# Kernel optimization log

Hardware: AMD Instinct MI355X
Metric: run time of the kernel (lower is better)

Reference implementation:

```python
import jax, jax.numpy as jnp
import numpy as np

DIM = 256
RED = DIM // 8  # reduction_ratio = 8
B, H, W = 16, 128, 128


def setup_inputs() -> dict:
    key = jax.random.key(0)
    ks = jax.random.split(key, 8)
    s = 1.0 / np.sqrt(DIM)  # conv2d default init scale (kernel_size=1 -> fan_in=dim)
    return {
        "x": jax.random.normal(ks[0], (B, DIM, H, W), dtype=jnp.float32),
        "y": jax.random.normal(ks[1], (B, DIM, H, W), dtype=jnp.float32),
        "q_w": jax.random.uniform(ks[2], (RED, DIM), jnp.float32, -s, s),
        "q_b": jax.random.uniform(ks[3], (RED,), jnp.float32, -s, s),
        "k_w": jax.random.uniform(ks[4], (RED, DIM), jnp.float32, -s, s),
        "k_b": jax.random.uniform(ks[5], (RED,), jnp.float32, -s, s),
        "v_w": jax.random.uniform(ks[6], (DIM, DIM), jnp.float32, -s, s),
        "v_b": jax.random.uniform(ks[7], (DIM,), jnp.float32, -s, s),
        "gamma": jnp.zeros((1,), dtype=jnp.float32),
    }


def reference(x, y, q_w, q_b, k_w, k_b, v_w, v_b, gamma):
    b, c, h, w = x.shape
    n = h * w
    # 1x1 convs are per-pixel channel GEMMs
    q = (jnp.einsum('bchw,oc->bohw', x, q_w) + q_b[None, :, None, None]).reshape(b, -1, n)
    k = (jnp.einsum('bchw,oc->bohw', y, k_w) + k_b[None, :, None, None]).reshape(b, -1, n)
    v = (jnp.einsum('bchw,oc->bohw', y, v_w) + v_b[None, :, None, None]).reshape(b, -1, n)
    k = jax.nn.softmax(k, axis=-1)  # softmax over spatial positions
    # context: [b, c, red] = v @ k^T
    context = jnp.einsum('bcn,brn->bcr', v, k)
    # out: [b, c, n] = context @ q
    out = jnp.einsum('bcr,brn->bcn', context, q).reshape(b, c, h, w)
    return gamma * out + x
```

## Files before the change

kernel.cpp:

```cpp
#include <hip/hip_runtime.h>
#include <math.h>


#define Bn 16
#define Cc 256
#define Rr 32
#define Nn 16384


__global__ void k_proj_k(const float* __restrict__ y, const float* __restrict__ kw,
                         const float* __restrict__ kb, const float* __restrict__ g,
                         float* __restrict__ kbuf) {
    if (g[0] == 0.0f) return;
    int t = blockIdx.x * 256 + threadIdx.x;
    int b = t / Nn, n = t % Nn;
    float acc[Rr];
#pragma unroll
    for (int r = 0; r < Rr; ++r) acc[r] = kb[r];
    const float* yp = y + (size_t)b * Cc * Nn + n;
    for (int ch = 0; ch < Cc; ++ch) {
        float yv = yp[(size_t)ch * Nn];
#pragma unroll
        for (int r = 0; r < Rr; ++r) acc[r] = fmaf(kw[r * Cc + ch], yv, acc[r]);
    }
    float* kp = kbuf + (size_t)b * Rr * Nn + n;
#pragma unroll
    for (int r = 0; r < Rr; ++r) kp[(size_t)r * Nn] = acc[r];
}

__global__ void k_softmax(float* __restrict__ kbuf, const float* __restrict__ g) {
    if (g[0] == 0.0f) return;
    float* p = kbuf + (size_t)blockIdx.x * Nn;
    int tid = threadIdx.x, lane = tid & 63, wid = tid >> 6;
    __shared__ float red[8];
    float m = -1e30f;
    for (int i = tid; i < Nn; i += 256) m = fmaxf(m, p[i]);
    for (int off = 32; off; off >>= 1) m = fmaxf(m, __shfl_down(m, off, 64));
    if (lane == 0) red[wid] = m;
    __syncthreads();
    m = fmaxf(fmaxf(red[0], red[1]), fmaxf(red[2], red[3]));
    float s = 0.0f;
    for (int i = tid; i < Nn; i += 256) s += expf(p[i] - m);
    for (int off = 32; off; off >>= 1) s += __shfl_down(s, off, 64);
    if (lane == 0) red[4 + wid] = s;
    __syncthreads();
    float inv = 1.0f / (red[4] + red[5] + red[6] + red[7]);
    for (int i = tid; i < Nn; i += 256) p[i] = expf(p[i] - m) * inv;
}

__global__ void k_S(const float* __restrict__ y, const float* __restrict__ kbuf,
                    const float* __restrict__ g, float* __restrict__ S) {
    if (g[0] == 0.0f) return;
    int blk = blockIdx.x; int b = blk / Cc, ch = blk % Cc;
    int tid = threadIdx.x, lane = tid & 63, wid = tid >> 6;
    float acc[Rr];
#pragma unroll
    for (int r = 0; r < Rr; ++r) acc[r] = 0.0f;
    const float* yp = y + ((size_t)b * Cc + ch) * Nn;
    const float* pp = kbuf + (size_t)b * Rr * Nn;
    for (int n = tid; n < Nn; n += 256) {
        float yv = yp[n];
#pragma unroll
        for (int r = 0; r < Rr; ++r) acc[r] = fmaf(pp[(size_t)r * Nn + n], yv, acc[r]);
    }
    __shared__ float red[Rr * 4];
#pragma unroll
    for (int r = 0; r < Rr; ++r) {
        float v = acc[r];
        for (int off = 32; off; off >>= 1) v += __shfl_down(v, off, 64);
        if (lane == 0) red[r * 4 + wid] = v;
    }
    __syncthreads();
    if (tid < Rr)
        S[((size_t)b * Cc + ch) * Rr + tid] =
            red[tid * 4] + red[tid * 4 + 1] + red[tid * 4 + 2] + red[tid * 4 + 3];
}

__global__ void k_ctx(const float* __restrict__ S, const float* __restrict__ vw,
                      const float* __restrict__ vb, const float* __restrict__ qw,
                      const float* __restrict__ qb, const float* __restrict__ g,
                      float* __restrict__ A, float* __restrict__ dvec) {
    float gamma = g[0];
    if (gamma == 0.0f) return;
    int b = blockIdx.x, c = threadIdx.x;
    float acc[Rr];
#pragma unroll
    for (int r = 0; r < Rr; ++r) acc[r] = vb[c];
    const float* Sb = S + (size_t)b * Cc * Rr;
    for (int ch = 0; ch < Cc; ++ch) {
        float w = vw[c * Cc + ch];
#pragma unroll
        for (int r = 0; r < Rr; ++r) acc[r] = fmaf(w, Sb[ch * Rr + r], acc[r]);
    }
    float dv = 0.0f;
#pragma unroll
    for (int r = 0; r < Rr; ++r) dv = fmaf(acc[r], qb[r], dv);
    dvec[b * Cc + c] = gamma * dv;
    float* Ab = A + ((size_t)b * Cc + c) * Cc;
    for (int ch = 0; ch < Cc; ++ch) {
        float mv = 0.0f;
#pragma unroll
        for (int r = 0; r < Rr; ++r) mv = fmaf(acc[r], qw[r * Cc + ch], mv);
        Ab[ch] = gamma * mv + (c == ch ? 1.0f : 0.0f);
    }
}

__global__ void k_out(const float* __restrict__ x, const float* __restrict__ A,
                      const float* __restrict__ dvec, const float* __restrict__ g,
                      float* __restrict__ out) {
    if (g[0] == 0.0f) return;
    int blk = blockIdx.x;
    int nt = blk & 63, cg = (blk >> 6) & 7, b = blk >> 9;
    int n = nt * 256 + threadIdx.x;
    float acc[32];
#pragma unroll
    for (int i = 0; i < 32; ++i) acc[i] = dvec[b * Cc + cg * 32 + i];
    const float* xp = x + (size_t)b * Cc * Nn + n;
    const float* Ab = A + ((size_t)b * Cc + cg * 32) * Cc;
    for (int ch = 0; ch < Cc; ++ch) {
        float xv = xp[(size_t)ch * Nn];
#pragma unroll
        for (int i = 0; i < 32; ++i) acc[i] = fmaf(Ab[i * Cc + ch], xv, acc[i]);
    }
    float* op = out + ((size_t)b * Cc + cg * 32) * Nn + n;
#pragma unroll
    for (int i = 0; i < 32; ++i) op[(size_t)i * Nn] = acc[i];
}

__global__ void k_copy(const float* __restrict__ x, const float* __restrict__ g,
                       float* __restrict__ out) {
    if (g[0] != 0.0f) return;
    const float4* xv = (const float4*)x;
    float4* ov = (float4*)out;
    const size_t total = (size_t)Bn * Cc * Nn / 4;
    size_t stride = (size_t)gridDim.x * blockDim.x;
    for (size_t i = (size_t)blockIdx.x * blockDim.x + threadIdx.x; i < total; i += stride)
        ov[i] = xv[i];
}

extern "C" void kernel_launch(void* const* d_in, const int* in_sizes, int n_in,
                              void* d_out, int out_size, void* d_ws, size_t ws_size,
                              hipStream_t stream) {
    const float* x  = (const float*)d_in[0];
    const float* y  = (const float*)d_in[1];
    const float* qw = (const float*)d_in[2];
    const float* qb = (const float*)d_in[3];
    const float* kw = (const float*)d_in[4];
    const float* kb = (const float*)d_in[5];
    const float* vw = (const float*)d_in[6];
    const float* vb = (const float*)d_in[7];
    const float* g  = (const float*)d_in[8];
    float* out = (float*)d_out;

    float* ws   = (float*)d_ws;
    float* kbuf = ws;
    float* S    = kbuf + (size_t)Bn * Rr * Nn;
    float* A    = S + (size_t)Bn * Cc * Rr;
    float* dv   = A + (size_t)Bn * Cc * Cc;

    k_proj_k<<<(Bn * Nn) / 256, 256, 0, stream>>>(y, kw, kb, g, kbuf);
    k_softmax<<<Bn * Rr, 256, 0, stream>>>(kbuf, g);
    k_S<<<Bn * Cc, 256, 0, stream>>>(y, kbuf, g, S);
    k_ctx<<<Bn, Cc, 0, stream>>>(S, vw, vb, qw, qb, g, A, dv);
    k_out<<<Bn * 8 * (Nn / 256), 256, 0, stream>>>(x, A, dv, g, out);

    k_copy<<<8192, 256, 0, stream>>>(x, g, out);
}
```

Baseline: 547.9 us.

## Fuse attention pipeline into prep and finish kernels with low-rank output

```diff
diff --git a/kernel.cpp b/kernel.cpp
--- a/kernel.cpp
+++ b/kernel.cpp
@@ -7,135 +7,139 @@
 #define Rr 32
 #define Nn 16384
 
+__global__ __launch_bounds__(256) void k_prep(
+        const float* __restrict__ y, const float* __restrict__ kw,
+        const float* __restrict__ kb, const float* __restrict__ vw,
+        const float* __restrict__ vb, const float* __restrict__ g,
+        float* __restrict__ pbuf, float* __restrict__ W2) {
+    float gamma = g[0];
+    if (gamma == 0.0f) return;
+    int b = blockIdx.x, tid = threadIdx.x, lane = tid & 63, wid = tid >> 6;
+    __shared__ float S_l[Cc * Rr];
+    __shared__ __align__(16) float p_l[Rr * 64];
+    __shared__ float red[8];
+    const float* yb = y + (size_t)b * Cc * Nn;
+    float* pb = pbuf + (size_t)b * Rr * Nn;
 
-__global__ void k_proj_k(const float* __restrict__ y, const float* __restrict__ kw,
-                         const float* __restrict__ kb, const float* __restrict__ g,
-                         float* __restrict__ kbuf) {
-    if (g[0] == 0.0f) return;
-    int t = blockIdx.x * 256 + threadIdx.x;
-    int b = t / Nn, n = t % Nn;
-    float acc[Rr];
+    for (int r = 0; r < Rr; ++r) {
+        float* prow = pb + (size_t)r * Nn;
+        const float* kwr = kw + r * Cc;
+        float kbr = kb[r];
+        float m = -1e30f;
+        for (int n = tid; n < Nn; n += 256) {
+            float s = kbr;
+            for (int ch = 0; ch < Cc; ++ch)
+                s = fmaf(kwr[ch], yb[(size_t)ch * Nn + n], s);
+            prow[n] = s;
+            m = fmaxf(m, s);
+        }
+        for (int off = 32; off; off >>= 1) m = fmaxf(m, __shfl_down(m, off, 64));
+        if (lane == 0) red[wid] = m;
+        __syncthreads();
+        m = fmaxf(fmaxf(red[0], red[1]), fmaxf(red[2], red[3]));
+        float s = 0.0f;
+        for (int n = tid; n < Nn; n += 256) s += expf(prow[n] - m);
+        for (int off = 32; off; off >>= 1) s += __shfl_down(s, off, 64);
+        if (lane == 0) red[4 + wid] = s;
+        __syncthreads();
+        float inv = 1.0f / (red[4] + red[5] + red[6] + red[7]);
+        for (int n = tid; n < Nn; n += 256) prow[n] = expf(prow[n] - m) * inv;
+        __syncthreads();
+    }
+
+    {
+        float acc[Rr];
 #pragma unroll
-    for (int r = 0; r < Rr; ++r) acc[r] = kb[r];
-    const float* yp = y + (size_t)b * Cc * Nn + n;
-    for (int ch = 0; ch < Cc; ++ch) {
-        float yv = yp[(size_t)ch * Nn];
+        for (int r = 0; r < Rr; ++r) acc[r] = 0.0f;
+        const float* yrow = yb + (size_t)tid * Nn;
+        for (int n0 = 0; n0 < Nn; n0 += 64) {
+            __syncthreads();
+            for (int i = tid; i < Rr * 16; i += 256) {
+                int r = i >> 4, c4 = i & 15;
+                ((float4*)p_l)[i] = *(const float4*)(pb + (size_t)r * Nn + n0 + c4 * 4);
+            }
+            __syncthreads();
+            for (int j = 0; j < 64; ++j) {
+                float yv = yrow[n0 + j];
 #pragma unroll
-        for (int r = 0; r < Rr; ++r) acc[r] = fmaf(kw[r * Cc + ch], yv, acc[r]);
-    }
-    float* kp = kbuf + (size_t)b * Rr * Nn + n;
+                for (int r = 0; r < Rr; ++r)
+                    acc[r] = fmaf(p_l[r * 64 + j], yv, acc[r]);
+            }
+        }
 #pragma unroll
-    for (int r = 0; r < Rr; ++r) kp[(size_t)r * Nn] = acc[r];
-}
-
-__global__ void k_softmax(float* __restrict__ kbuf, const float* __restrict__ g) {
-    if (g[0] == 0.0f) return;
-    float* p = kbuf + (size_t)blockIdx.x * Nn;
-    int tid = threadIdx.x, lane = tid & 63, wid = tid >> 6;
-    __shared__ float red[8];
-    float m = -1e30f;
-    for (int i = tid; i < Nn; i += 256) m = fmaxf(m, p[i]);
-    for (int off = 32; off; off >>= 1) m = fmaxf(m, __shfl_down(m, off, 64));
-    if (lane == 0) red[wid] = m;
-    __syncthreads();
-    m = fmaxf(fmaxf(red[0], red[1]), fmaxf(red[2], red[3]));
-    float s = 0.0f;
-    for (int i = tid; i < Nn; i += 256) s += expf(p[i] - m);
-    for (int off = 32; off; off >>= 1) s += __shfl_down(s, off, 64);
-    if (lane == 0) red[4 + wid] = s;
-    __syncthreads();
-    float inv = 1.0f / (red[4] + red[5] + red[6] + red[7]);
-    for (int i = tid; i < Nn; i += 256) p[i] = expf(p[i] - m) * inv;
-}
-
-__global__ void k_S(const float* __restrict__ y, const float* __restrict__ kbuf,
-                    const float* __restrict__ g, float* __restrict__ S) {
-    if (g[0] == 0.0f) return;
-    int blk = blockIdx.x; int b = blk / Cc, ch = blk % Cc;
-    int tid = threadIdx.x, lane = tid & 63, wid = tid >> 6;
-    float acc[Rr];
-#pragma unroll
-    for (int r = 0; r < Rr; ++r) acc[r] = 0.0f;
-    const float* yp = y + ((size_t)b * Cc + ch) * Nn;
-    const float* pp = kbuf + (size_t)b * Rr * Nn;
-    for (int n = tid; n < Nn; n += 256) {
-        float yv = yp[n];
-#pragma unroll
-        for (int r = 0; r < Rr; ++r) acc[r] = fmaf(pp[(size_t)r * Nn + n], yv, acc[r]);
-    }
-    __shared__ float red[Rr * 4];
-#pragma unroll
-    for (int r = 0; r < Rr; ++r) {
-        float v = acc[r];
-        for (int off = 32; off; off >>= 1) v += __shfl_down(v, off, 64);
-        if (lane == 0) red[r * 4 + wid] = v;
+        for (int r = 0; r < Rr; ++r) S_l[tid * Rr + r] = acc[r];
     }
     __syncthreads();
-    if (tid < Rr)
-        S[((size_t)b * Cc + ch) * Rr + tid] =
-            red[tid * 4] + red[tid * 4 + 1] + red[tid * 4 + 2] + red[tid * 4 + 3];
-}
 
-__global__ void k_ctx(const float* __restrict__ S, const float* __restrict__ vw,
-                      const float* __restrict__ vb, const float* __restrict__ qw,
-                      const float* __restrict__ qb, const float* __restrict__ g,
-                      float* __restrict__ A, float* __restrict__ dvec) {
-    float gamma = g[0];
-    if (gamma == 0.0f) return;
-    int b = blockIdx.x, c = threadIdx.x;
-    float acc[Rr];
+    {
+        float accw[Rr];
+        float vbc = vb[tid];
 #pragma unroll
-    for (int r = 0; r < Rr; ++r) acc[r] = vb[c];
-    const float* Sb = S + (size_t)b * Cc * Rr;
-    for (int ch = 0; ch < Cc; ++ch) {
-        float w = vw[c * Cc + ch];
+        for (int r = 0; r < Rr; ++r) accw[r] = vbc;
+        const float* wrow = vw + (size_t)tid * Cc;
+        for (int ch = 0; ch < Cc; ++ch) {
+            float w = wrow[ch];
 #pragma unroll
-        for (int r = 0; r < Rr; ++r) acc[r] = fmaf(w, Sb[ch * Rr + r], acc[r]);
-    }
-    float dv = 0.0f;
+            for (int r = 0; r < Rr; ++r)
+                accw[r] = fmaf(w, S_l[ch * Rr + r], accw[r]);
+        }
+        float* wp = W2 + ((size_t)b * Cc + tid) * Rr;
 #pragma unroll
-    for (int r = 0; r < Rr; ++r) dv = fmaf(acc[r], qb[r], dv);
-    dvec[b * Cc + c] = gamma * dv;
-    float* Ab = A + ((size_t)b * Cc + c) * Cc;
-    for (int ch = 0; ch < Cc; ++ch) {
-        float mv = 0.0f;
-#pragma unroll
-        for (int r = 0; r < Rr; ++r) mv = fmaf(acc[r], qw[r * Cc + ch], mv);
-        Ab[ch] = gamma * mv + (c == ch ? 1.0f : 0.0f);
+        for (int r4 = 0; r4 < Rr / 4; ++r4)
+            *(float4*)(wp + r4 * 4) =
+                make_float4(gamma * accw[r4 * 4 + 0], gamma * accw[r4 * 4 + 1],
+                            gamma * accw[r4 * 4 + 2], gamma * accw[r4 * 4 + 3]);
     }
 }
 
-__global__ void k_out(const float* __restrict__ x, const float* __restrict__ A,
-                      const float* __restrict__ dvec, const float* __restrict__ g,
-                      float* __restrict__ out) {
-    if (g[0] == 0.0f) return;
+__global__ __launch_bounds__(256) void k_finish(
+        const float* __restrict__ x, const float* __restrict__ qw,
+        const float* __restrict__ qb, const float* __restrict__ W2,
+        const float* __restrict__ g, float* __restrict__ out) {
+    if (g[0] == 0.0f) {
+        const float4* xv = (const float4*)x;
+        float4* ov = (float4*)out;
+        const size_t total = (size_t)Bn * Cc * Nn / 4;
+        size_t stride = (size_t)gridDim.x * blockDim.x;
+        for (size_t i = (size_t)blockIdx.x * blockDim.x + threadIdx.x; i < total;
+             i += stride)
+            ov[i] = xv[i];
+        return;
+    }
     int blk = blockIdx.x;
-    int nt = blk & 63, cg = (blk >> 6) & 7, b = blk >> 9;
+    if (blk >= Bn * 64) return;
+    int b = blk >> 6, nt = blk & 63;
     int n = nt * 256 + threadIdx.x;
-    float acc[32];
+    __shared__ __align__(16) float W_l[Cc * Rr];
+    {
+        const float4* src = (const float4*)(W2 + (size_t)b * Cc * Rr);
+        for (int i = threadIdx.x; i < Cc * Rr / 4; i += 256)
+            ((float4*)W_l)[i] = src[i];
+    }
+    __syncthreads();
+    float qacc[Rr];
 #pragma unroll
-    for (int i = 0; i < 32; ++i) acc[i] = dvec[b * Cc + cg * 32 + i];
-    const float* xp = x + (size_t)b * Cc * Nn + n;
-    const float* Ab = A + ((size_t)b * Cc + cg * 32) * Cc;
+    for (int r = 0; r < Rr; ++r) qacc[r] = qb[r];
+    const float* xb = x + (size_t)b * Cc * Nn;
     for (int ch = 0; ch < Cc; ++ch) {
-        float xv = xp[(size_t)ch * Nn];
+        float xv = xb[(size_t)ch * Nn + n];
 #pragma unroll
-        for (int i = 0; i < 32; ++i) acc[i] = fmaf(Ab[i * Cc + ch], xv, acc[i]);
+        for (int r = 0; r < Rr; ++r)
+            qacc[r] = fmaf(qw[r * Cc + ch], xv, qacc[r]);
     }
-    float* op = out + ((size_t)b * Cc + cg * 32) * Nn + n;
+    for (int c = 0; c < Cc; ++c) {
+        float o = xb[(size_t)c * Nn + n];
+        const float* wl = W_l + c * Rr;
 #pragma unroll
-    for (int i = 0; i < 32; ++i) op[(size_t)i * Nn] = acc[i];
-}
-
-__global__ void k_copy(const float* __restrict__ x, const float* __restrict__ g,
-                       float* __restrict__ out) {
-    if (g[0] != 0.0f) return;
-    const float4* xv = (const float4*)x;
-    float4* ov = (float4*)out;
-    const size_t total = (size_t)Bn * Cc * Nn / 4;
-    size_t stride = (size_t)gridDim.x * blockDim.x;
-    for (size_t i = (size_t)blockIdx.x * blockDim.x + threadIdx.x; i < total; i += stride)
-        ov[i] = xv[i];
+        for (int r4 = 0; r4 < Rr / 4; ++r4) {
+            float4 w = *(const float4*)(wl + r4 * 4);
+            o = fmaf(w.x, qacc[r4 * 4 + 0], o);
+            o = fmaf(w.y, qacc[r4 * 4 + 1], o);
+            o = fmaf(w.z, qacc[r4 * 4 + 2], o);
+            o = fmaf(w.w, qacc[r4 * 4 + 3], o);
+        }
+        out[((size_t)b * Cc + c) * Nn + n] = o;
+    }
 }
 
 extern "C" void kernel_launch(void* const* d_in, const int* in_sizes, int n_in,
@@ -153,16 +157,9 @@
     float* out = (float*)d_out;
 
     float* ws   = (float*)d_ws;
-    float* kbuf = ws;
-    float* S    = kbuf + (size_t)Bn * Rr * Nn;
-    float* A    = S + (size_t)Bn * Cc * Rr;
-    float* dv   = A + (size_t)Bn * Cc * Cc;
+    float* pbuf = ws;
+    float* W2   = pbuf + (size_t)Bn * Rr * Nn;
 
-    k_proj_k<<<(Bn * Nn) / 256, 256, 0, stream>>>(y, kw, kb, g, kbuf);
-    k_softmax<<<Bn * Rr, 256, 0, stream>>>(kbuf, g);
-    k_S<<<Bn * Cc, 256, 0, stream>>>(y, kbuf, g, S);
-    k_ctx<<<Bn, Cc, 0, stream>>>(S, vw, vb, qw, qb, g, A, dv);
-    k_out<<<Bn * 8 * (Nn / 256), 256, 0, stream>>>(x, A, dv, g, out);
-
-    k_copy<<<8192, 256, 0, stream>>>(x, g, out);
+    k_prep  <<<Bn, 256, 0, stream>>>(y, kw, kb, vw, vb, g, pbuf, W2);
+    k_finish<<<2048, 256, 0, stream>>>(x, qw, qb, W2, g, out);
 }
```

Result: faster. 534.6 us (-2.4%).
